# Performance work log

Hardware: AMD Instinct MI355X
Metric: run time of the kernel (lower is better)

## Reference

```python
import jax, jax.numpy as jnp
import numpy as np

B, N, L = 16, 128, 512            # batch, scan length, per-step feature (= configs.seq_len)
D, S, K, R, H = 1024, 16, 4, 64, 2048  # d_model, d_state, ker_size, dt_rank, hidden_dimention


def _mamba_params(key, scale=0.02):
    ks = jax.random.split(key, 6)
    return dict(
        in_w=jax.random.normal(ks[0], (2 * D, L)) * scale,
        conv_w=jax.random.normal(ks[1], (D, K)) * scale,
        conv_b=jnp.zeros((D,)),
        xproj_w=jax.random.normal(ks[2], (R + 2 * S, D)) * scale,
        dt_w=jax.random.normal(ks[3], (D, R)) * scale,
        dt_b=jax.random.normal(ks[4], (D,)) * scale,
        A_log=jnp.tile(jnp.log(jnp.arange(1, S + 1, dtype=jnp.float32)), (D, 1)),
        Dp=jnp.ones((D,)),
        out_w=jax.random.normal(ks[5], (L, D)) * scale,
    )


def setup_inputs():
    key = jax.random.key(0)
    kx, kf, kr, k1, k2 = jax.random.split(key, 5)
    inp = {"x": jax.random.normal(kx, (B, N, L), dtype=jnp.float32)}
    for pre, k in (("f_", kf), ("r_", kr)):
        for n, v in _mamba_params(k).items():
            inp[pre + n] = v
    inp["pu_w"] = jax.random.normal(k1, (H, L)) * 0.02
    inp["pu_b"] = jnp.zeros((H,))
    inp["pl_w"] = jax.random.normal(k2, (L, H)) * 0.02
    inp["pl_b"] = jnp.zeros((L,))
    inp["ln_g"] = jnp.ones((L,))
    inp["ln_b"] = jnp.zeros((L,))
    return inp


def _ln(x, g, b, eps=1e-5):
    m = x.mean(-1, keepdims=True)
    v = ((x - m) ** 2).mean(-1, keepdims=True)
    return (x - m) * jax.lax.rsqrt(v + eps) * g + b


def _dw_causal_conv(x, w, b):
    # x: [B,N,D]; depthwise causal conv along N with kernel [D,K]
    xt = jnp.pad(x.transpose(0, 2, 1), ((0, 0), (0, 0), (K - 1, 0)))  # [B,D,N+K-1]
    y = jax.lax.conv_general_dilated(xt, w[:, None, :], (1,), 'VALID',
                                     dimension_numbers=('NCH', 'OIH', 'NCH'),
                                     feature_group_count=D)
    return (y + b[None, :, None]).transpose(0, 2, 1)


def _mamba(x, in_w, conv_w, conv_b, xproj_w, dt_w, dt_b, A_log, Dp, out_w):
    # standard Mamba block (in_proj -> depthwise conv -> silu -> selective scan -> gate -> out_proj)
    xi, res = jnp.split(x @ in_w.T, 2, axis=-1)             # [B,N,D] each
    xc = jax.nn.silu(_dw_causal_conv(xi, conv_w, conv_b))   # [B,N,D]
    dbc = xc @ xproj_w.T                                    # [B,N,R+2S]
    dt, Bm, Cm = dbc[..., :R], dbc[..., R:R + S], dbc[..., R + S:]
    delta = jax.nn.softplus(dt @ dt_w.T + dt_b)             # [B,N,D]
    A = -jnp.exp(A_log)                                     # [D,S]
    dA = jnp.exp(delta[..., None] * A)                      # [B,N,D,S]
    dBx = delta[..., None] * Bm[:, :, None, :] * xc[..., None]

    def step(h, t):
        dA_t, dBx_t, C_t = t
        h = dA_t * h + dBx_t                                # [B,D,S]
        return h, jnp.einsum('bds,bs->bd', h, C_t)

    _, ys = jax.lax.scan(step, jnp.zeros((x.shape[0], D, S), x.dtype),
                         (dA.transpose(1, 0, 2, 3), dBx.transpose(1, 0, 2, 3), Cm.transpose(1, 0, 2)))
    y = ys.transpose(1, 0, 2) + xc * Dp                     # [B,N,D]
    y = y * jax.nn.silu(res)
    return y @ out_w.T                                      # [B,N,L]


def reference(x, f_in_w, f_conv_w, f_conv_b, f_xproj_w, f_dt_w, f_dt_b, f_A_log, f_Dp, f_out_w,
              r_in_w, r_conv_w, r_conv_b, r_xproj_w, r_dt_w, r_dt_b, r_A_log, r_Dp, r_out_w,
              pu_w, pu_b, pl_w, pl_b, ln_g, ln_b):
    y1 = _mamba(x, f_in_w, f_conv_w, f_conv_b, f_xproj_w, f_dt_w, f_dt_b, f_A_log, f_Dp, f_out_w)
    y2 = _mamba(x[:, ::-1, :], r_in_w, r_conv_w, r_conv_b, r_xproj_w, r_dt_w, r_dt_b, r_A_log, r_Dp, r_out_w)
    y3 = _ln(x + y1 + y2[:, ::-1, :], ln_g, ln_b)
    yp = jax.nn.relu(y3 @ pu_w.T + pu_b)
    yp = yp @ pl_w.T + pl_b
    return _ln(yp + y3, ln_g, ln_b)
```

## Files before the change

kernel.cpp:

```cpp
#include <hip/hip_runtime.h>
#include <hip/hip_bf16.h>
#include <cstdint>

typedef __hip_bfloat16 bf16;

constexpr int Bb = 16, Nn = 128, Ll = 512, Dd = 1024, Ss = 16, Rr = 64, Hh = 2048;
constexpr int Mm = Bb * Nn;
#define LOG2E 1.44269504088896340736f

using bf16x8 = __attribute__((ext_vector_type(8))) __bf16;
using bf16x4 = __attribute__((ext_vector_type(4))) __bf16;
using f32x4  = __attribute__((ext_vector_type(4))) float;

__device__ __forceinline__ float to_f(float x) { return x; }
__device__ __forceinline__ float to_f(bf16 x) { return __bfloat162float(x); }
__device__ __forceinline__ void store_t(float* p, float v) { *p = v; }
__device__ __forceinline__ void store_t(bf16* p, float v) { *p = __float2bfloat16(v); }
__device__ __forceinline__ __bf16 cvt1(float x) {
  bf16 h = __float2bfloat16(x);
  return *reinterpret_cast<__bf16*>(&h);
}
__device__ __forceinline__ float bfraw_to_f(__bf16 x) {
  bf16 h = *reinterpret_cast<bf16*>(&x);
  return __bfloat162float(h);
}
__device__ __forceinline__ bf16x8 load8(const bf16* p) { return *(const bf16x8*)p; }
__device__ __forceinline__ bf16x8 load8(const float* p) {
  float4 a = *(const float4*)p;
  float4 b = *(const float4*)(p + 4);
  bf16x8 r;
  r[0] = cvt1(a.x); r[1] = cvt1(a.y); r[2] = cvt1(a.z); r[3] = cvt1(a.w);
  r[4] = cvt1(b.x); r[5] = cvt1(b.y); r[6] = cvt1(b.z); r[7] = cvt1(b.w);
  return r;
}
__device__ __forceinline__ bf16x8 load8rt(const void* p, size_t idx, int isbf) {
  if (isbf) return load8((const bf16*)p + idx);
  return load8((const float*)p + idx);
}
__device__ __forceinline__ float ldf(const void* p, int i, int isbf) {
  if (isbf) return __bfloat162float(((const bf16*)p)[i]);
  return ((const float*)p)[i];
}
__device__ __forceinline__ void gld16(const bf16* g, __bf16* l) {
  __builtin_amdgcn_global_load_lds(
      (const __attribute__((address_space(1))) void*)g,
      (__attribute__((address_space(3))) void*)l, 16, 0, 0);
}

enum { EPI_STORE = 0, EPI_BIAS_RELU = 1, EPI_ADD = 3, EPI_BIAS = 4, EPI_BIAS_SOFTPLUS = 5,
       EPI_ATOMIC = 6 };

__global__ void sniff_kernel(const unsigned short* __restrict__ xs, int* __restrict__ flags) {
  const int tid = threadIdx.x;
  int cnt = 0;
  for (int j = 0; j < 64; ++j) {
    int i = tid + j * 256;
    unsigned short u = xs[(size_t)i * 64];
    bf16 h = *reinterpret_cast<bf16*>(&u);
    float v = __bfloat162float(h);
    float a = fabsf(v);
    if (v == 0.f || (a > 0.0009765625f && a < 16.f)) ++cnt;
  }
  __shared__ int sc[256];
  sc[tid] = cnt;
  __syncthreads();
  for (int o = 128; o > 0; o >>= 1) {
    if (tid < o) sc[tid] += sc[tid + o];
    __syncthreads();
  }
  if (tid == 0) flags[0] = (sc[0] > 8192) ? 1 : 0;
}

__global__ __launch_bounds__(256) void prep_kernel(
    const int* __restrict__ flagp, const void* __restrict__ x,
    float* __restrict__ ZB, unsigned short* __restrict__ Xb,
    float* __restrict__ zerop,
    const void* __restrict__ fin, const void* __restrict__ rin,
    const void* __restrict__ fout, const void* __restrict__ rout,
    const void* __restrict__ puw, const void* __restrict__ plw,
    bf16* __restrict__ WBin, bf16* __restrict__ WBout,
    bf16* __restrict__ WBpu, bf16* __restrict__ WBpl) {
  const int isbf = *flagp;
  const int i = blockIdx.x * 256 + threadIdx.x;
  if (i < 262144) {
    float4 o;
    ushort4 u;
    if (isbf) {
      u = ((const ushort4*)x)[i];
      bf16 h0 = *reinterpret_cast<bf16*>(&u.x), h1 = *reinterpret_cast<bf16*>(&u.y);
      bf16 h2 = *reinterpret_cast<bf16*>(&u.z), h3 = *reinterpret_cast<bf16*>(&u.w);
      o = float4{__bfloat162float(h0), __bfloat162float(h1),
                 __bfloat162float(h2), __bfloat162float(h3)};
    } else {
      o = ((const float4*)x)[i];
      bf16 h0 = __float2bfloat16(o.x), h1 = __float2bfloat16(o.y);
      bf16 h2 = __float2bfloat16(o.z), h3 = __float2bfloat16(o.w);
      u = ushort4{*(unsigned short*)&h0, *(unsigned short*)&h1,
                  *(unsigned short*)&h2, *(unsigned short*)&h3};
    }
    ((float4*)ZB)[i] = o;
    ((ushort4*)Xb)[i] = u;
  } else if (i < 622592) {
    ((float4*)zerop)[i - 262144] = float4{0.f, 0.f, 0.f, 0.f};
  } else {
    const int j = i - 622592;
    const void* src;
    bf16* dst;
    int si;
    if (j < 131072) { src = fin; si = j; dst = WBin + (size_t)si * 8; }
    else if (j < 262144) { src = rin; si = j - 131072; dst = WBin + (size_t)1048576 + (size_t)si * 8; }
    else if (j < 393216) { src = puw; si = j - 262144; dst = WBpu + (size_t)si * 8; }
    else if (j < 524288) { src = plw; si = j - 393216; dst = WBpl + (size_t)si * 8; }
    else if (j < 589824) {
      src = fout; si = j - 524288;
      int e = si * 8;
      dst = WBout + (size_t)(e >> 10) * 2048 + (e & 1023);
    } else {
      src = rout; si = j - 589824;
      int e = si * 8;
      dst = WBout + (size_t)(e >> 10) * 2048 + 1024 + (e & 1023);
    }
    *(bf16x8*)dst = load8rt(src, (size_t)si * 8, isbf);
  }
}

constexpr int LDT2 = 72;

template <typename TC, int EPI>
__global__ __launch_bounds__(256) void gemm_rt(
    const int* __restrict__ flagp,
    const void* __restrict__ A, int lda, int abf,
    const void* __restrict__ Bw, const void* __restrict__ Bw2, int ldb,
    int bmode, int bsplit,
    TC* __restrict__ C, int ldc,
    const void* __restrict__ bias, const void* __restrict__ bias2,
    int N, int Kchunk, int zk, size_t a_doff, size_t c_doff) {
  const int isbf = *flagp;
  const int ab = (abf == 2) ? isbf : abf;
  __shared__ __align__(16) __bf16 As[64 * LDT2];
  __shared__ __align__(16) __bf16 Bs[64 * LDT2];
  const int tid = threadIdx.x;
  const int wave = tid >> 6, lane = tid & 63;
  const int quad = lane >> 4, l16 = lane & 15;
  const int wm = wave & 1, wn = wave >> 1;
  int bx = blockIdx.x, by = blockIdx.y;
  const int gx = gridDim.x, gy = gridDim.y;
  if ((gx & 7) == 0) {
    int id = bx + gx * by;
    int xcd = id & 7, sl = id >> 3;
    by = sl % gy;
    bx = (sl / gy) * 8 + xcd;
  }
  int zsl = blockIdx.z;
  const void* Ap = A;
  const void* Bp0 = Bw;
  const void* biasp = bias;
  if (bmode == 3) {
    const int dir = zsl / zk;
    zsl = zsl % zk;
    if (dir) {
      Ap = (const char*)A + a_doff * (size_t)(ab ? 2 : 4);
      C += c_doff;
      Bp0 = Bw2;
      biasp = bias2;
    }
  }
  const int m0 = by * 64, n0 = bx * 64;
  const int kb = zsl * Kchunk;
  const int srow = tid >> 3;
  const int scol = (tid & 7) * 8;
  f32x4 acc[2][2] = {};
  for (int k0 = kb; k0 < kb + Kchunk; k0 += 64) {
#pragma unroll
    for (int h = 0; h < 2; ++h) {
      int r = srow + h * 32;
      *(bf16x8*)(&As[r * LDT2 + scol]) =
          load8rt(Ap, (size_t)(m0 + r) * lda + k0 + scol, ab);
      int rb = n0 + r;
      rb = rb < N ? rb : N - 1;
      size_t bi = (size_t)rb * ldb + k0 + scol;
      *(bf16x8*)(&Bs[r * LDT2 + scol]) = load8rt(Bp0, bi, isbf);
    }
    __syncthreads();
#pragma unroll
    for (int kk2 = 0; kk2 < 2; ++kk2) {
      bf16x8 af[2], bfr[2];
#pragma unroll
      for (int i = 0; i < 2; ++i)
        af[i] = *(const bf16x8*)(&As[(wm * 32 + i * 16 + l16) * LDT2 + kk2 * 32 + quad * 8]);
#pragma unroll
      for (int j = 0; j < 2; ++j)
        bfr[j] = *(const bf16x8*)(&Bs[(wn * 32 + j * 16 + l16) * LDT2 + kk2 * 32 + quad * 8]);
#pragma unroll
      for (int i = 0; i < 2; ++i)
#pragma unroll
        for (int j = 0; j < 2; ++j)
          acc[i][j] = __builtin_amdgcn_mfma_f32_16x16x32_bf16(af[i], bfr[j], acc[i][j], 0, 0, 0);
    }
    __syncthreads();
  }
#pragma unroll
  for (int i = 0; i < 2; ++i) {
#pragma unroll
    for (int j = 0; j < 2; ++j) {
      const int col = n0 + wn * 32 + j * 16 + l16;
      if (col >= N) continue;
      float bv = 0.f;
      if (EPI == EPI_BIAS_RELU || EPI == EPI_BIAS || EPI == EPI_BIAS_SOFTPLUS)
        bv = ldf(biasp, col, isbf);
#pragma unroll
      for (int r = 0; r < 4; ++r) {
        const int row = m0 + wm * 32 + i * 16 + quad * 4 + r;
        size_t idx = (size_t)row * ldc + col;
        float v = acc[i][j][r];
        if (EPI == EPI_STORE) store_t(&C[idx], v);
        else if (EPI == EPI_BIAS_RELU) { v += bv; store_t(&C[idx], v > 0.f ? v : 0.f); }
        else if (EPI == EPI_BIAS) store_t(&C[idx], v + bv);
        else if (EPI == EPI_BIAS_SOFTPLUS) {
          v += bv;
          store_t(&C[idx], (v > 20.f) ? v : log1pf(__expf(v)));
        } else if (EPI == EPI_ATOMIC) {
          atomicAdd((float*)&C[idx], v);
        }
      }
    }
  }
}

template <typename TC, int EPI>
__global__ __launch_bounds__(256) void gemm128n(
    const int* __restrict__ flagp,
    const bf16* __restrict__ A, int lda,
    const bf16* __restrict__ Bw, int ldb,
    TC* __restrict__ C, int ldc,
    const void* __restrict__ bias,
    int Kchunk) {
  __shared__ __align__(16) __bf16 As[2][128 * 64];
  __shared__ __align__(16) __bf16 Bs[2][128 * 64];
  const int tid = threadIdx.x;
  const int wave = tid >> 6, lane = tid & 63;
  const int quad = lane >> 4, l16 = lane & 15;
  const int wr = wave >> 1, wc = wave & 1;
  int bx = blockIdx.x, by = blockIdx.y;
  const int gx = gridDim.x, gy = gridDim.y;
  if ((gx & 7) == 0) {
    int id = bx + gx * by;
    int xcd = id & 7, sl = id >> 3;
    by = sl % gy;
    bx = (sl / gy) * 8 + xcd;
  }
  const int m0 = by * 128, n0 = bx * 128;
  const int kb = blockIdx.z * Kchunk;
  const int kend = kb + Kchunk;
  const int lr = lane >> 3;
  const int lc = (lane & 7) * 8;
  auto STAGE = [&](int buf, int k0) {
#pragma unroll
    for (int rr = 0; rr < 4; ++rr) {
      const int rowb = rr * 32 + wave * 8;
      gld16(A + (size_t)(m0 + rowb + lr) * lda + k0 + lc, &As[buf][rowb * 64]);
      gld16(Bw + (size_t)(n0 + rowb + lr) * ldb + k0 + lc, &Bs[buf][rowb * 64]);
    }
  };
  f32x4 acc[4][4] = {};
  int cur = 0;
  STAGE(0, kb);
  __syncthreads();
  for (int k0 = kb; k0 < kend; k0 += 64) {
    if (k0 + 64 < kend) STAGE(cur ^ 1, k0 + 64);
#pragma unroll
    for (int kk = 0; kk < 2; ++kk) {
      bf16x8 af[4], bfr[4];
#pragma unroll
      for (int i = 0; i < 4; ++i)
        af[i] = *(const bf16x8*)(&As[cur][(wr * 64 + i * 16 + l16) * 64 + kk * 32 + quad * 8]);
#pragma unroll
      for (int j = 0; j < 4; ++j)
        bfr[j] = *(const bf16x8*)(&Bs[cur][(wc * 64 + j * 16 + l16) * 64 + kk * 32 + quad * 8]);
#pragma unroll
      for (int i = 0; i < 4; ++i)
#pragma unroll
        for (int j = 0; j < 4; ++j)
          acc[i][j] = __builtin_amdgcn_mfma_f32_16x16x32_bf16(af[i], bfr[j], acc[i][j], 0, 0, 0);
    }
    __syncthreads();
    cur ^= 1;
  }
  const int isbf = *flagp;
#pragma unroll
  for (int i = 0; i < 4; ++i) {
#pragma unroll
    for (int j = 0; j < 4; ++j) {
      const int col = n0 + wc * 64 + j * 16 + l16;
      float bv = 0.f;
      if (EPI == EPI_BIAS_RELU) bv = ldf(bias, col, isbf);
#pragma unroll
      for (int r = 0; r < 4; ++r) {
        const int row = m0 + wr * 64 + i * 16 + quad * 4 + r;
        size_t idx = (size_t)row * ldc + col;
        float v = acc[i][j][r];
        if (EPI == EPI_STORE) store_t(&C[idx], v);
        else if (EPI == EPI_BIAS_RELU) { v += bv; store_t(&C[idx], v > 0.f ? v : 0.f); }
        else if (EPI == EPI_ATOMIC) atomicAdd((float*)&C[idx], v);
      }
    }
  }
}

__global__ __launch_bounds__(256) void conv_silu_rt(
    const int* __restrict__ flagp, const bf16* __restrict__ X2b,
    const void* __restrict__ fcw, const void* __restrict__ fcb,
    const void* __restrict__ rcw, const void* __restrict__ rcb,
    bf16* __restrict__ XCb) {
  const int isbf = *flagp;
  const int dir = blockIdx.y >> 2;
  const int d = (blockIdx.y & 3) * 256 + threadIdx.x;
  const int m = blockIdx.x;
  const int t = m & (Nn - 1);
  const void* cw = dir ? rcw : fcw;
  const void* cb = dir ? rcb : fcb;
  float w0 = ldf(cw, d * 4 + 0, isbf), w1 = ldf(cw, d * 4 + 1, isbf);
  float w2 = ldf(cw, d * 4 + 2, isbf), w3 = ldf(cw, d * 4 + 3, isbf);
  float a = ldf(cb, d, isbf);
  const size_t base = (size_t)m * 4096 + (size_t)dir * 2048 + d;
  if (dir == 0) {
    if (t >= 3) a += w0 * to_f(X2b[base - 3 * 4096]);
    if (t >= 2) a += w1 * to_f(X2b[base - 2 * 4096]);
    if (t >= 1) a += w2 * to_f(X2b[base - 1 * 4096]);
    a += w3 * to_f(X2b[base]);
  } else {
    if (t + 3 < Nn) a += w0 * to_f(X2b[base + 3 * 4096]);
    if (t + 2 < Nn) a += w1 * to_f(X2b[base + 2 * 4096]);
    if (t + 1 < Nn) a += w2 * to_f(X2b[base + 1 * 4096]);
    a += w3 * to_f(X2b[base]);
  }
  const float s = a / (1.f + __builtin_amdgcn_exp2f(-a * LOG2E));
  XCb[(size_t)m * 2048 + (size_t)dir * 1024 + d] = __float2bfloat16(s);
}

__global__ __launch_bounds__(128) void scan_gate3(
    const int* __restrict__ flagp,
    const float* __restrict__ DBC0, bf16* __restrict__ XCb, const bf16* __restrict__ X2b,
    const bf16* __restrict__ DELTA0,
    const void* __restrict__ fAlog, const void* __restrict__ fDp,
    const void* __restrict__ rAlog, const void* __restrict__ rDp) {
  const int isbf = *flagp;
  const int dir = blockIdx.z;
  const float* DBC = DBC0 + (size_t)dir * Mm * 96;
  const bf16* DELTA = DELTA0 + (size_t)dir * Mm * 1024;
  const void* A_log = dir ? rAlog : fAlog;
  const void* Dp = dir ? rDp : fDp;
  __shared__ __align__(16) __bf16 sBC[Nn * 32];
  __shared__ __align__(16) __bf16 sD[Nn * 32];
  __shared__ __align__(16) __bf16 sX[Nn * 32];
  __shared__ __align__(16) __bf16 sG[Nn * 32];
  const int b = blockIdx.x;
  const int d0 = blockIdx.y * 32;
  const int tid = threadIdx.x;
  const size_t rowbase = (size_t)b * Nn;
  const size_t xc_col = (size_t)dir * 1024;
#pragma unroll
  for (int k = 0; k < 8; ++k) {
    int idx = tid + k * 128;
    int t = idx >> 3, c = idx & 7;
    float4 v = *(const float4*)(DBC + (rowbase + t) * 96 + 64 + c * 4);
    bf16x4 pv = {cvt1(v.x), cvt1(v.y), cvt1(v.z), cvt1(v.w)};
    int dst = (c < 4) ? (t * 32 + c * 8) : (t * 32 + (c - 4) * 8 + 4);
    *(bf16x4*)&sBC[dst] = pv;
  }
#pragma unroll
  for (int k = 0; k < 4; ++k) {
    int idx = tid + k * 128;
    int t = idx >> 2, h = idx & 3;
    *(uint4*)&sD[t * 32 + h * 8] =
        *(const uint4*)(DELTA + (rowbase + t) * 1024 + d0 + h * 8);
    *(uint4*)&sX[t * 32 + h * 8] =
        *(const uint4*)(XCb + (rowbase + t) * 2048 + xc_col + d0 + h * 8);
    bf16x8 rv = *(const bf16x8*)(X2b + (rowbase + t) * 4096 + (size_t)dir * 2048 + 1024 + d0 + h * 8);
    bf16x8 gv;
#pragma unroll
    for (int e = 0; e < 8; ++e) {
      float r = bfraw_to_f(rv[e]);
      gv[e] = cvt1(r / (1.f + __builtin_amdgcn_exp2f(-r * LOG2E)));
    }
    *(bf16x8*)&sG[t * 32 + h * 8] = gv;
  }
  __syncthreads();
  const int wv = tid >> 6, lane = tid & 63;
  const int dl = lane & 15, sg = lane >> 4;
  const int d_local = wv * 16 + dl;
  const int d = d0 + d_local;
  float A_[4];
#pragma unroll
  for (int j = 0; j < 4; ++j)
    A_[j] = -__expf(ldf(A_log, d * Ss + sg * 4 + j, isbf)) * LOG2E;
  const float dp = ldf(Dp, d, isbf);
  float h0 = 0.f, h1 = 0.f, h2 = 0.f, h3 = 0.f;
  for (int pg = 0; pg < Nn / 4; ++pg) {
    float accs[4], xvs[4];
#pragma unroll
    for (int u = 0; u < 4; ++u) {
      const int p = pg * 4 + u;
      const int t = dir ? (Nn - 1 - p) : p;
      const float dv = bfraw_to_f(sD[t * 32 + d_local]);
      const float xv = bfraw_to_f(sX[t * 32 + d_local]);
      bf16x8 bc = *(const bf16x8*)&sBC[t * 32 + sg * 8];
      const float dx = dv * xv;
      h0 = __builtin_amdgcn_exp2f(dv * A_[0]) * h0 + dx * bfraw_to_f(bc[0]);
      h1 = __builtin_amdgcn_exp2f(dv * A_[1]) * h1 + dx * bfraw_to_f(bc[1]);
      h2 = __builtin_amdgcn_exp2f(dv * A_[2]) * h2 + dx * bfraw_to_f(bc[2]);
      h3 = __builtin_amdgcn_exp2f(dv * A_[3]) * h3 + dx * bfraw_to_f(bc[3]);
      accs[u] = h0 * bfraw_to_f(bc[4]) + h1 * bfraw_to_f(bc[5]) +
                h2 * bfraw_to_f(bc[6]) + h3 * bfraw_to_f(bc[7]);
      xvs[u] = xv;
    }
#pragma unroll
    for (int u = 0; u < 4; ++u) {
      float a = accs[u];
      a += __shfl_xor(a, 16, 64);
      a += __shfl_xor(a, 32, 64);
      if (sg == 0) {
        const int p = pg * 4 + u;
        const int t = dir ? (Nn - 1 - p) : p;
        const float g = bfraw_to_f(sG[t * 32 + d_local]);
        XCb[(rowbase + t) * 2048 + xc_col + d] = __float2bfloat16((a + xvs[u] * dp) * g);
      }
    }
  }
}

template <int MODE>
__global__ __launch_bounds__(256) void ln_rt(const int* __restrict__ flagp,
                                             const float* __restrict__ Z,
                                             const float* __restrict__ Zadd,
                                             const void* __restrict__ g,
                                             const void* __restrict__ bb,
                                             const void* __restrict__ pb,
                                             void* __restrict__ outp,
                                             bf16* __restrict__ outp2) {
  const int isbf = *flagp;
  const int row = blockIdx.x;
  const int tid = threadIdx.x;
  const int c0 = tid * 2;
  const float2* z = (const float2*)(Z + (size_t)row * Ll);
  float2 v = z[tid];
  if (MODE == 1) {
    const float2* za = (const float2*)(Zadd + (size_t)row * Ll);
    float2 a = za[tid];
    v.x += a.x + ldf(pb, c0, isbf);
    v.y += a.y + ldf(pb, c0 + 1, isbf);
  }
  float s = v.x + v.y, q = v.x * v.x + v.y * v.y;
#pragma unroll
  for (int o = 32; o > 0; o >>= 1) {
    s += __shfl_xor(s, o, 64);
    q += __shfl_xor(q, o, 64);
  }
  __shared__ float ss[4], qq[4];
  const int wv = tid >> 6, ln = tid & 63;
  if (ln == 0) { ss[wv] = s; qq[wv] = q; }
  __syncthreads();
  s = ss[0] + ss[1] + ss[2] + ss[3];
  q = qq[0] + qq[1] + qq[2] + qq[3];
  const float mean = s * (1.f / Ll);
  const float var = q * (1.f / Ll) - mean * mean;
  const float rs = rsqrtf(var + 1e-5f);
  const float o0 = (v.x - mean) * rs * ldf(g, c0, isbf) + ldf(bb, c0, isbf);
  const float o1 = (v.y - mean) * rs * ldf(g, c0 + 1, isbf) + ldf(bb, c0 + 1, isbf);
  if (MODE == 0) {
    float* out = (float*)outp;
    out[(size_t)row * Ll + c0] = o0;
    out[(size_t)row * Ll + c0 + 1] = o1;
    outp2[(size_t)row * Ll + c0] = __float2bfloat16(o0);
    outp2[(size_t)row * Ll + c0 + 1] = __float2bfloat16(o1);
  } else {
    if (isbf) {
      bf16* out = (bf16*)outp;
      out[(size_t)row * Ll + c0] = __float2bfloat16(o0);
      out[(size_t)row * Ll + c0 + 1] = __float2bfloat16(o1);
    } else {
      float* out = (float*)outp;
      out[(size_t)row * Ll + c0] = o0;
      out[(size_t)row * Ll + c0 + 1] = o1;
    }
  }
}

extern "C" void kernel_launch(void* const* d_in, const int* in_sizes, int n_in, void* d_out,
                              int out_size, void* d_ws, size_t ws_size, hipStream_t stream) {
  char* ws = (char*)d_ws;
  int* flags = (int*)ws;
  bf16* X2b = (bf16*)(ws + 256);
  bf16* XCb = X2b + (size_t)Mm * 4096;
  bf16* Y3b = XCb + (size_t)Mm * 2048;
  bf16* DELTA = Y3b + (size_t)Mm * 512;
  bf16* Xb = DELTA + (size_t)2 * Mm * 1024;
  bf16* WBin = Xb + (size_t)Mm * 512;
  bf16* WBout = WBin + (size_t)4096 * 512;
  bf16* WBpu = WBout + (size_t)512 * 2048;
  bf16* WBpl = WBpu + (size_t)2048 * 512;
  float* DBC = (float*)(WBpl + (size_t)512 * 2048);
  float* Z2 = DBC + (size_t)2 * Mm * 96;
  float* ZB = Z2 + (size_t)Mm * 512;
  float* Y3 = ZB + (size_t)Mm * 512;
  bf16* H1 = X2b;
  size_t needed = 256 +
                  2 * ((size_t)Mm * 4096 + (size_t)Mm * 2048 + (size_t)Mm * 512 +
                       (size_t)2 * Mm * 1024 + (size_t)Mm * 512 +
                       (size_t)4096 * 512 + (size_t)512 * 2048 +
                       (size_t)2048 * 512 + (size_t)512 * 2048) +
                  4 * ((size_t)2 * Mm * 96 + (size_t)3 * Mm * 512);
  if (ws_size < needed) return;

  const void* x = d_in[0];
  const dim3 blk(256);

  sniff_kernel<<<dim3(1), blk, 0, stream>>>((const unsigned short*)x, flags);
  prep_kernel<<<dim3(4992), blk, 0, stream>>>(
      flags, x, ZB, (unsigned short*)Xb, DBC,
      d_in[1], d_in[10], d_in[9], d_in[18], d_in[19], d_in[21],
      WBin, WBout, WBpu, WBpl);
  gemm128n<bf16, EPI_STORE><<<dim3(32, 16), blk, 0, stream>>>(
      flags, Xb, Ll, WBin, Ll, X2b, 4096, nullptr, Ll);
  conv_silu_rt<<<dim3(Mm, 8), blk, 0, stream>>>(flags, X2b, d_in[2], d_in[3],
                                                d_in[11], d_in[12], XCb);
  gemm_rt<float, EPI_ATOMIC><<<dim3(2, 32, 8), blk, 0, stream>>>(
      flags, XCb, 2048, 1, d_in[4], d_in[13], Dd, 3, 0,
      DBC, 96, nullptr, nullptr, 96, 256, 4, 1024, (size_t)Mm * 96);
  gemm_rt<bf16, EPI_BIAS_SOFTPLUS><<<dim3(16, 32, 2), blk, 0, stream>>>(
      flags, DBC, 96, 0, d_in[5], d_in[14], Rr, 3, 0,
      DELTA, 1024, d_in[6], d_in[15], 1024, Rr, 1, (size_t)Mm * 96, (size_t)Mm * 1024);
  scan_gate3<<<dim3(Bb, Dd / 32, 2), dim3(128), 0, stream>>>(
      flags, DBC, XCb, X2b, DELTA, d_in[7], d_in[8], d_in[16], d_in[17]);
  gemm128n<float, EPI_ATOMIC><<<dim3(4, 16, 4), blk, 0, stream>>>(
      flags, XCb, 2048, WBout, 2048, ZB, Ll, nullptr, Ll);
  ln_rt<0><<<dim3(Mm), blk, 0, stream>>>(flags, ZB, nullptr, d_in[23], d_in[24], nullptr,
                                         (void*)Y3, Y3b);
  gemm128n<bf16, EPI_BIAS_RELU><<<dim3(16, 16), blk, 0, stream>>>(
      flags, Y3b, Ll, WBpu, Ll, H1, Hh, d_in[20], Ll);
  gemm128n<float, EPI_ATOMIC><<<dim3(4, 16, 4), blk, 0, stream>>>(
      flags, H1, Hh, WBpl, 2048, Z2, Ll, nullptr, Ll);
  ln_rt<1><<<dim3(Mm), blk, 0, stream>>>(flags, Z2, Y3, d_in[23], d_in[24], d_in[22],
                                         d_out, nullptr);

  (void)in_sizes; (void)n_in; (void)out_size;
}
```

Baseline: 336.5 us.

## Split scan state across eight lanes per channel with 256-thread blocks

The selective-scan kernel now spreads each channel's 16 state elements over 8 lanes holding 2 states each, instead of 4 lanes holding 4, and doubles the block to 256 threads so each block still covers 32 channels. The shared B/C layout is re-interleaved so each lane reads one 4-element vector of its B and C pairs. The aim is to shorten the serial dependency chain per thread and raise wave-level parallelism for this latency-bound recurrence. The cost is an extra cross-lane shuffle per output and more redundant per-lane loads of delta and x.

```diff
diff --git a/kernel.cpp b/kernel.cpp
--- a/kernel.cpp
+++ b/kernel.cpp
@@ -338,7 +338,7 @@
   XCb[(size_t)m * 2048 + (size_t)dir * 1024 + d] = __float2bfloat16(s);
 }
 
-__global__ __launch_bounds__(128) void scan_gate3(
+__global__ __launch_bounds__(256) void scan_gate5(
     const int* __restrict__ flagp,
     const float* __restrict__ DBC0, bf16* __restrict__ XCb, const bf16* __restrict__ X2b,
     const bf16* __restrict__ DELTA0,
@@ -360,17 +360,22 @@
   const size_t rowbase = (size_t)b * Nn;
   const size_t xc_col = (size_t)dir * 1024;
 #pragma unroll
-  for (int k = 0; k < 8; ++k) {
-    int idx = tid + k * 128;
+  for (int k = 0; k < 4; ++k) {
+    int idx = tid + k * 256;
     int t = idx >> 3, c = idx & 7;
     float4 v = *(const float4*)(DBC + (rowbase + t) * 96 + 64 + c * 4);
-    bf16x4 pv = {cvt1(v.x), cvt1(v.y), cvt1(v.z), cvt1(v.w)};
-    int dst = (c < 4) ? (t * 32 + c * 8) : (t * 32 + (c - 4) * 8 + 4);
-    *(bf16x4*)&sBC[dst] = pv;
-  }
-#pragma unroll
-  for (int k = 0; k < 4; ++k) {
-    int idx = tid + k * 128;
+    const int isC = (c >= 4) ? 2 : 0;
+    const int cb4 = (c & 3) * 4;
+    float vv[4] = {v.x, v.y, v.z, v.w};
+#pragma unroll
+    for (int e = 0; e < 4; ++e) {
+      int s = cb4 + e;
+      sBC[t * 32 + (s >> 1) * 4 + isC + (s & 1)] = cvt1(vv[e]);
+    }
+  }
+#pragma unroll
+  for (int k = 0; k < 2; ++k) {
+    int idx = tid + k * 256;
     int t = idx >> 2, h = idx & 3;
     *(uint4*)&sD[t * 32 + h * 8] =
         *(const uint4*)(DELTA + (rowbase + t) * 1024 + d0 + h * 8);
@@ -387,15 +392,13 @@
   }
   __syncthreads();
   const int wv = tid >> 6, lane = tid & 63;
-  const int dl = lane & 15, sg = lane >> 4;
-  const int d_local = wv * 16 + dl;
+  const int dl = lane & 7, sgp = lane >> 3;
+  const int d_local = wv * 8 + dl;
   const int d = d0 + d_local;
-  float A_[4];
-#pragma unroll
-  for (int j = 0; j < 4; ++j)
-    A_[j] = -__expf(ldf(A_log, d * Ss + sg * 4 + j, isbf)) * LOG2E;
+  float A0 = -__expf(ldf(A_log, d * Ss + sgp * 2 + 0, isbf)) * LOG2E;
+  float A1 = -__expf(ldf(A_log, d * Ss + sgp * 2 + 1, isbf)) * LOG2E;
   const float dp = ldf(Dp, d, isbf);
-  float h0 = 0.f, h1 = 0.f, h2 = 0.f, h3 = 0.f;
+  float h0 = 0.f, h1 = 0.f;
   for (int pg = 0; pg < Nn / 4; ++pg) {
     float accs[4], xvs[4];
 #pragma unroll
@@ -404,22 +407,20 @@
       const int t = dir ? (Nn - 1 - p) : p;
       const float dv = bfraw_to_f(sD[t * 32 + d_local]);
       const float xv = bfraw_to_f(sX[t * 32 + d_local]);
-      bf16x8 bc = *(const bf16x8*)&sBC[t * 32 + sg * 8];
+      bf16x4 bc = *(const bf16x4*)&sBC[t * 32 + sgp * 4];
       const float dx = dv * xv;
-      h0 = __builtin_amdgcn_exp2f(dv * A_[0]) * h0 + dx * bfraw_to_f(bc[0]);
-      h1 = __builtin_amdgcn_exp2f(dv * A_[1]) * h1 + dx * bfraw_to_f(bc[1]);
-      h2 = __builtin_amdgcn_exp2f(dv * A_[2]) * h2 + dx * bfraw_to_f(bc[2]);
-      h3 = __builtin_amdgcn_exp2f(dv * A_[3]) * h3 + dx * bfraw_to_f(bc[3]);
-      accs[u] = h0 * bfraw_to_f(bc[4]) + h1 * bfraw_to_f(bc[5]) +
-                h2 * bfraw_to_f(bc[6]) + h3 * bfraw_to_f(bc[7]);
+      h0 = __builtin_amdgcn_exp2f(dv * A0) * h0 + dx * bfraw_to_f(bc[0]);
+      h1 = __builtin_amdgcn_exp2f(dv * A1) * h1 + dx * bfraw_to_f(bc[1]);
+      accs[u] = h0 * bfraw_to_f(bc[2]) + h1 * bfraw_to_f(bc[3]);
       xvs[u] = xv;
     }
 #pragma unroll
     for (int u = 0; u < 4; ++u) {
       float a = accs[u];
+      a += __shfl_xor(a, 8, 64);
       a += __shfl_xor(a, 16, 64);
       a += __shfl_xor(a, 32, 64);
-      if (sg == 0) {
+      if (sgp == 0) {
         const int p = pg * 4 + u;
         const int t = dir ? (Nn - 1 - p) : p;
         const float g = bfraw_to_f(sG[t * 32 + d_local]);
@@ -530,7 +531,7 @@
   gemm_rt<bf16, EPI_BIAS_SOFTPLUS><<<dim3(16, 32, 2), blk, 0, stream>>>(
       flags, DBC, 96, 0, d_in[5], d_in[14], Rr, 3, 0,
       DELTA, 1024, d_in[6], d_in[15], 1024, Rr, 1, (size_t)Mm * 96, (size_t)Mm * 1024);
-  scan_gate3<<<dim3(Bb, Dd / 32, 2), dim3(128), 0, stream>>>(
+  scan_gate5<<<dim3(Bb, Dd / 32, 2), blk, 0, stream>>>(
       flags, DBC, XCb, X2b, DELTA, d_in[7], d_in[8], d_in[16], d_in[17]);
   gemm128n<float, EPI_ATOMIC><<<dim3(4, 16, 4), blk, 0, stream>>>(
       flags, XCb, 2048, WBout, 2048, ZB, Ll, nullptr, Ll);
```

Measured after the change: 320.4 us. 4.8% less time.

## Remap scan lanes to quads, reduce with DPP, stage outputs through LDS

Applied to the files above, without the earlier changes.

The selective-scan kernel now gives each 256-thread block 64 channels instead of 32, and lays out the four state groups of a channel in adjacent lanes. The per-step state reduction then uses quad DPP moves rather than cross-row shuffles. Outputs are written to an LDS tile and stored to global memory in coalesced 16-byte vectors after the scan, replacing scattered 2-byte stores. The cost is more LDS per block, which may lower occupancy, plus an extra barrier and copy pass at the end.

```diff
diff --git a/kernel.cpp b/kernel.cpp
--- a/kernel.cpp
+++ b/kernel.cpp
@@ -46,6 +46,19 @@
       (const __attribute__((address_space(1))) void*)g,
       (__attribute__((address_space(3))) void*)l, 16, 0, 0);
 }
+#if __has_builtin(__builtin_amdgcn_mov_dpp)
+__device__ __forceinline__ float quad_xor1(float v) {
+  int r = __builtin_amdgcn_mov_dpp(__builtin_bit_cast(int, v), 0xB1, 0xF, 0xF, true);
+  return __builtin_bit_cast(float, r);
+}
+__device__ __forceinline__ float quad_xor2(float v) {
+  int r = __builtin_amdgcn_mov_dpp(__builtin_bit_cast(int, v), 0x4E, 0xF, 0xF, true);
+  return __builtin_bit_cast(float, r);
+}
+#else
+__device__ __forceinline__ float quad_xor1(float v) { return __shfl_xor(v, 1, 64); }
+__device__ __forceinline__ float quad_xor2(float v) { return __shfl_xor(v, 2, 64); }
+#endif
 
 enum { EPI_STORE = 0, EPI_BIAS_RELU = 1, EPI_ADD = 3, EPI_BIAS = 4, EPI_BIAS_SOFTPLUS = 5,
        EPI_ATOMIC = 6 };
@@ -338,7 +351,7 @@
   XCb[(size_t)m * 2048 + (size_t)dir * 1024 + d] = __float2bfloat16(s);
 }
 
-__global__ __launch_bounds__(128) void scan_gate3(
+__global__ __launch_bounds__(256) void scan_gate8(
     const int* __restrict__ flagp,
     const float* __restrict__ DBC0, bf16* __restrict__ XCb, const bf16* __restrict__ X2b,
     const bf16* __restrict__ DELTA0,
@@ -351,17 +364,18 @@
   const void* A_log = dir ? rAlog : fAlog;
   const void* Dp = dir ? rDp : fDp;
   __shared__ __align__(16) __bf16 sBC[Nn * 32];
-  __shared__ __align__(16) __bf16 sD[Nn * 32];
-  __shared__ __align__(16) __bf16 sX[Nn * 32];
-  __shared__ __align__(16) __bf16 sG[Nn * 32];
+  __shared__ __align__(16) __bf16 sD[Nn * 64];
+  __shared__ __align__(16) __bf16 sX[Nn * 64];
+  __shared__ __align__(16) __bf16 sG[Nn * 64];
+  __shared__ __align__(16) __bf16 sY[Nn * 64];
   const int b = blockIdx.x;
-  const int d0 = blockIdx.y * 32;
+  const int d0 = blockIdx.y * 64;
   const int tid = threadIdx.x;
   const size_t rowbase = (size_t)b * Nn;
   const size_t xc_col = (size_t)dir * 1024;
 #pragma unroll
-  for (int k = 0; k < 8; ++k) {
-    int idx = tid + k * 128;
+  for (int k = 0; k < 4; ++k) {
+    int idx = tid + k * 256;
     int t = idx >> 3, c = idx & 7;
     float4 v = *(const float4*)(DBC + (rowbase + t) * 96 + 64 + c * 4);
     bf16x4 pv = {cvt1(v.x), cvt1(v.y), cvt1(v.z), cvt1(v.w)};
@@ -370,11 +384,11 @@
   }
 #pragma unroll
   for (int k = 0; k < 4; ++k) {
-    int idx = tid + k * 128;
-    int t = idx >> 2, h = idx & 3;
-    *(uint4*)&sD[t * 32 + h * 8] =
+    int idx = tid + k * 256;
+    int t = idx >> 3, h = idx & 7;
+    *(uint4*)&sD[t * 64 + h * 8] =
         *(const uint4*)(DELTA + (rowbase + t) * 1024 + d0 + h * 8);
-    *(uint4*)&sX[t * 32 + h * 8] =
+    *(uint4*)&sX[t * 64 + h * 8] =
         *(const uint4*)(XCb + (rowbase + t) * 2048 + xc_col + d0 + h * 8);
     bf16x8 rv = *(const bf16x8*)(X2b + (rowbase + t) * 4096 + (size_t)dir * 2048 + 1024 + d0 + h * 8);
     bf16x8 gv;
@@ -383,11 +397,11 @@
       float r = bfraw_to_f(rv[e]);
       gv[e] = cvt1(r / (1.f + __builtin_amdgcn_exp2f(-r * LOG2E)));
     }
-    *(bf16x8*)&sG[t * 32 + h * 8] = gv;
+    *(bf16x8*)&sG[t * 64 + h * 8] = gv;
   }
   __syncthreads();
   const int wv = tid >> 6, lane = tid & 63;
-  const int dl = lane & 15, sg = lane >> 4;
+  const int sg = lane & 3, dl = lane >> 2;
   const int d_local = wv * 16 + dl;
   const int d = d0 + d_local;
   float A_[4];
@@ -402,8 +416,8 @@
     for (int u = 0; u < 4; ++u) {
       const int p = pg * 4 + u;
       const int t = dir ? (Nn - 1 - p) : p;
-      const float dv = bfraw_to_f(sD[t * 32 + d_local]);
-      const float xv = bfraw_to_f(sX[t * 32 + d_local]);
+      const float dv = bfraw_to_f(sD[t * 64 + d_local]);
+      const float xv = bfraw_to_f(sX[t * 64 + d_local]);
       bf16x8 bc = *(const bf16x8*)&sBC[t * 32 + sg * 8];
       const float dx = dv * xv;
       h0 = __builtin_amdgcn_exp2f(dv * A_[0]) * h0 + dx * bfraw_to_f(bc[0]);
@@ -417,15 +431,23 @@
 #pragma unroll
     for (int u = 0; u < 4; ++u) {
       float a = accs[u];
-      a += __shfl_xor(a, 16, 64);
-      a += __shfl_xor(a, 32, 64);
+      a += quad_xor1(a);
+      a += quad_xor2(a);
       if (sg == 0) {
         const int p = pg * 4 + u;
         const int t = dir ? (Nn - 1 - p) : p;
-        const float g = bfraw_to_f(sG[t * 32 + d_local]);
-        XCb[(rowbase + t) * 2048 + xc_col + d] = __float2bfloat16((a + xvs[u] * dp) * g);
+        const float g = bfraw_to_f(sG[t * 64 + d_local]);
+        sY[t * 64 + d_local] = cvt1((a + xvs[u] * dp) * g);
       }
     }
+  }
+  __syncthreads();
+#pragma unroll
+  for (int k = 0; k < 4; ++k) {
+    int idx = tid + k * 256;
+    int t = idx >> 3, h = idx & 7;
+    *(uint4*)(XCb + (rowbase + t) * 2048 + xc_col + d0 + h * 8) =
+        *(const uint4*)&sY[t * 64 + h * 8];
   }
 }
 
@@ -530,7 +552,7 @@
   gemm_rt<bf16, EPI_BIAS_SOFTPLUS><<<dim3(16, 32, 2), blk, 0, stream>>>(
       flags, DBC, 96, 0, d_in[5], d_in[14], Rr, 3, 0,
       DELTA, 1024, d_in[6], d_in[15], 1024, Rr, 1, (size_t)Mm * 96, (size_t)Mm * 1024);
-  scan_gate3<<<dim3(Bb, Dd / 32, 2), dim3(128), 0, stream>>>(
+  scan_gate8<<<dim3(Bb, Dd / 64, 2), blk, 0, stream>>>(
       flags, DBC, XCb, X2b, DELTA, d_in[7], d_in[8], d_in[16], d_in[17]);
   gemm128n<float, EPI_ATOMIC><<<dim3(4, 16, 4), blk, 0, stream>>>(
       flags, XCb, 2048, WBout, 2048, ZB, Ll, nullptr, Ll);
```

After: 314.2 us. 6.6% less time.
